# Performance work log

Measured on AMD Instinct MI355X. Metric: run time of the kernel, lower is better.

Reference implementation:

```python
import jax, jax.numpy as jnp
import numpy as np

INPUT_SIZE = 512
HIDDEN_SIZE = 512
BATCH = 16384


def setup_inputs() -> dict:
    key = jax.random.key(0)
    ks = jax.random.split(key, 11)
    stdv = 1.0 / np.sqrt(HIDDEN_SIZE)
    in_dim = INPUT_SIZE + HIDDEN_SIZE

    def unif(k, shape):
        return jax.random.uniform(k, shape, jnp.float32, -stdv, stdv)

    inp = {
        "input_": jax.random.normal(ks[0], (BATCH, INPUT_SIZE), jnp.float32),
        "prev_h": jax.random.normal(ks[1], (BATCH, HIDDEN_SIZE), jnp.float32),
        "prev_c": jax.random.normal(ks[2], (BATCH, HIDDEN_SIZE), jnp.float32),
        # gate weights in torch nn.Linear layout: (out=hidden, in=input+hidden)
        "W_i": unif(ks[3], (HIDDEN_SIZE, in_dim)),
        "b_i": unif(ks[4], (HIDDEN_SIZE,)),
        "W_f": unif(ks[5], (HIDDEN_SIZE, in_dim)),
        "b_f": unif(ks[6], (HIDDEN_SIZE,)),
        "W_g": unif(ks[7], (HIDDEN_SIZE, in_dim)),
        "b_g": unif(ks[8], (HIDDEN_SIZE,)),
        "W_o": unif(ks[9], (HIDDEN_SIZE, in_dim)),
        "b_o": unif(ks[10], (HIDDEN_SIZE,)),
    }
    return inp


def reference(input_, prev_h, prev_c, W_i, b_i, W_f, b_f, W_g, b_g, W_o, b_o):
    # x_stack = cat((prev_h, input_), dim=1)  -> (batch, hidden+input)
    x_stack = jnp.concatenate([prev_h, input_], axis=1)
    # Fuse the four gate GEMMs into one: stack weights along out dim.
    W = jnp.concatenate([W_i, W_f, W_o, W_g], axis=0)          # (4H, H+I)
    b = jnp.concatenate([b_i, b_f, b_o, b_g], axis=0)          # (4H,)
    gates = x_stack @ W.T + b                                   # (batch, 4H)
    H = prev_h.shape[1]
    i = jax.nn.sigmoid(gates[:, 0 * H:1 * H])
    f = jax.nn.sigmoid(gates[:, 1 * H:2 * H])
    o = jax.nn.sigmoid(gates[:, 2 * H:3 * H])
    g = jnp.tanh(gates[:, 3 * H:4 * H])
    c = f * prev_c + i * g
    h = jnp.tanh(c) * o
    return (h, c)
```

## Files before the change

### kernel.cpp

```cpp
#include <hip/hip_runtime.h>
#include <hip/hip_bf16.h>
#include <math.h>

typedef unsigned short u16;

#define BATCH 16384
#define HID   512
#define KDIM  1024
#define BM    128
#define NSTEP 16

typedef __bf16 bf16x8 __attribute__((ext_vector_type(8)));
typedef float  floatx4 __attribute__((ext_vector_type(4)));

__device__ __forceinline__ float fast_sigmoid(float x) {
  return 1.0f / (1.0f + __expf(-x));
}
__device__ __forceinline__ float fast_tanh(float x) {
  float e = __expf(-2.0f * fabsf(x));
  float t = (1.0f - e) / (1.0f + e);
  return x >= 0.0f ? t : -t;
}
__device__ __forceinline__ u16 f2bf(float f) {
  return __builtin_bit_cast(u16, __float2bfloat16(f));
}

__device__ __forceinline__ void barrier_lds_only() {
  asm volatile("s_waitcnt lgkmcnt(0)" ::: "memory");
  __builtin_amdgcn_s_barrier();
  __builtin_amdgcn_sched_barrier(0);
}

__global__ __launch_bounds__(256) void pack_w_kernel(
    const float* __restrict__ Wi, const float* __restrict__ Wf_,
    const float* __restrict__ Wo, const float* __restrict__ Wg,
    u16* __restrict__ Wf) {
  int grow = blockIdx.x;
  int k = threadIdx.x * 4;
  int g = grow >> 9;
  int n = grow & (HID - 1);
  const float* s = g == 0 ? Wi : g == 1 ? Wf_ : g == 2 ? Wo : Wg;
  float4 v = *(const float4*)(s + (size_t)n * KDIM + k);
  ushort4 o;
  o.x = f2bf(v.x); o.y = f2bf(v.y); o.z = f2bf(v.z); o.w = f2bf(v.w);
  size_t d = ((size_t)((g * 32 + (n >> 4)) * 32 + (k >> 5)) * 64 +
              ((k >> 3) & 3) * 16 + (n & 15)) * 8 + (k & 7);
  *(ushort4*)(Wf + d) = o;
}

__global__ __launch_bounds__(512, 2) void lstm_gemm_kernel(
    const float* __restrict__ input_, const float* __restrict__ prev_h,
    const u16* __restrict__ Wf,
    const float* __restrict__ Bi, const float* __restrict__ Bf,
    const float* __restrict__ Bo, const float* __restrict__ Bg,
    const float* __restrict__ prevC, float* __restrict__ out) {
  __shared__ u16 lds[2][8192];

  const int tid = threadIdx.x;
  const int wave = tid >> 6, lane = tid & 63;
  const int lrow = lane & 15, lquad = lane >> 4;
  const int m_block = blockIdx.x * BM;
  const int ntg = blockIdx.y * 8 + wave;

  const int swzf = ((lane & 7) ^ ((lane >> 3) & 7)) * 8;
  const float* xh[2];
  const float* xi[2];
  int lp[2];
#pragma unroll
  for (int i = 0; i < 2; ++i) {
    int li = wave * 2 + i;
    int row = m_block + li * 8 + (lane >> 3);
    xh[i] = prev_h + (size_t)row * HID + swzf;
    xi[i] = input_ + (size_t)row * HID + swzf;
    lp[i] = li * 512 + lane * 8;
  }

  floatx4 acc[4][8];
#pragma unroll
  for (int g = 0; g < 4; ++g)
#pragma unroll
    for (int mt = 0; mt < 8; ++mt)
      acc[g][mt] = (floatx4){0.f, 0.f, 0.f, 0.f};

  float4 r[2][2];
  auto ldX = [&](int S) {
#pragma unroll
    for (int i = 0; i < 2; ++i) {
      const float* base = (S < 8) ? (xh[i] + S * 64) : (xi[i] + (S - 8) * 64);
      r[i][0] = *(const float4*)(base);
      r[i][1] = *(const float4*)(base + 4);
    }
  };

  auto cvtWrite = [&](int buf) {
#pragma unroll
    for (int i = 0; i < 2; ++i) {
      union { u16 u[8]; bf16x8 v; } t;
      t.u[0] = f2bf(r[i][0].x); t.u[1] = f2bf(r[i][0].y);
      t.u[2] = f2bf(r[i][0].z); t.u[3] = f2bf(r[i][0].w);
      t.u[4] = f2bf(r[i][1].x); t.u[5] = f2bf(r[i][1].y);
      t.u[6] = f2bf(r[i][1].z); t.u[7] = f2bf(r[i][1].w);
      *(bf16x8*)(&lds[buf][lp[i]]) = t.v;
    }
  };

  bf16x8 b[2][4];
  auto loadB = [&](int S) {
#pragma unroll
    for (int kk = 0; kk < 2; ++kk)
#pragma unroll
      for (int g = 0; g < 4; ++g)
        b[kk][g] = *(const bf16x8*)(
            Wf + (((size_t)(g * 32 + ntg) * 32 + (S * 2 + kk)) << 9) +
            lane * 8);
  };

  auto compute = [&](int buf) {
    const u16* LA = &lds[buf][0];
    __builtin_amdgcn_s_setprio(1);
#pragma unroll
    for (int kk = 0; kk < 2; ++kk) {
#pragma unroll
      for (int mt = 0; mt < 8; ++mt) {
        bf16x8 a = *(const bf16x8*)
            &LA[(mt * 16 + lrow) * 64 + (((kk * 4 + lquad) ^ (lrow & 7)) * 8)];
#pragma unroll
        for (int g = 0; g < 4; ++g)
          acc[g][mt] = __builtin_amdgcn_mfma_f32_16x16x32_bf16(
              a, b[kk][g], acc[g][mt], 0, 0, 0);
      }
    }
    __builtin_amdgcn_s_setprio(0);
  };

  loadB(0);
  ldX(0);
  cvtWrite(0);
  barrier_lds_only();

  for (int S = 0; S < NSTEP; ++S) {
    const int buf = S & 1;
    if (S + 1 < NSTEP) ldX(S + 1);
    compute(buf);
    if (S + 1 < NSTEP) {
      loadB(S + 1);
      cvtWrite(buf ^ 1);
      barrier_lds_only();
    }
  }

  const int j = ntg * 16 + lrow;
  const float vbi = Bi[j], vbf = Bf[j], vbo = Bo[j], vbg = Bg[j];
  float* outH = out;
  float* outC = out + (size_t)BATCH * HID;
#pragma unroll
  for (int mt = 0; mt < 8; ++mt) {
    int rowb = m_block + mt * 16 + lquad * 4;
#pragma unroll
    for (int rg = 0; rg < 4; ++rg) {
      int row = rowb + rg;
      float gi = fast_sigmoid(acc[0][mt][rg] + vbi);
      float gf = fast_sigmoid(acc[1][mt][rg] + vbf);
      float go = fast_sigmoid(acc[2][mt][rg] + vbo);
      float gg = fast_tanh(acc[3][mt][rg] + vbg);
      float c = gf * prevC[row * HID + j] + gi * gg;
      float h = fast_tanh(c) * go;
      outH[row * HID + j] = h;
      outC[row * HID + j] = c;
    }
  }
}

__global__ void lstm_fallback_kernel(
    const float* __restrict__ input_, const float* __restrict__ prev_h,
    const float* __restrict__ prevC,
    const float* __restrict__ Wi, const float* __restrict__ Bi,
    const float* __restrict__ Wf, const float* __restrict__ Bf,
    const float* __restrict__ Wo, const float* __restrict__ Bo,
    const float* __restrict__ Wg, const float* __restrict__ Bg,
    float* __restrict__ out) {
  int idx = blockIdx.x * blockDim.x + threadIdx.x;
  int b = idx / HID, j = idx % HID;
  if (b >= BATCH) return;
  float si = 0.f, sf = 0.f, so = 0.f, sg = 0.f;
  for (int k = 0; k < KDIM; ++k) {
    float x = (k < HID) ? prev_h[b * HID + k] : input_[b * HID + (k - HID)];
    si += x * Wi[j * KDIM + k];
    sf += x * Wf[j * KDIM + k];
    so += x * Wo[j * KDIM + k];
    sg += x * Wg[j * KDIM + k];
  }
  float gi = fast_sigmoid(si + Bi[j]);
  float gf = fast_sigmoid(sf + Bf[j]);
  float go = fast_sigmoid(so + Bo[j]);
  float gg = fast_tanh(sg + Bg[j]);
  float c = gf * prevC[b * HID + j] + gi * gg;
  out[b * HID + j] = fast_tanh(c) * go;
  out[(size_t)BATCH * HID + b * HID + j] = c;
}

extern "C" void kernel_launch(void* const* d_in, const int* in_sizes, int n_in,
                              void* d_out, int out_size, void* d_ws, size_t ws_size,
                              hipStream_t stream) {
  const float* input_ = (const float*)d_in[0];
  const float* prev_h = (const float*)d_in[1];
  const float* prev_c = (const float*)d_in[2];
  const float* W_i = (const float*)d_in[3];
  const float* b_i = (const float*)d_in[4];
  const float* W_f = (const float*)d_in[5];
  const float* b_f = (const float*)d_in[6];
  const float* W_g = (const float*)d_in[7];
  const float* b_g = (const float*)d_in[8];
  const float* W_o = (const float*)d_in[9];
  const float* b_o = (const float*)d_in[10];
  float* out = (float*)d_out;

  const size_t ws_needed = (size_t)4 * HID * KDIM * sizeof(u16);

  if (ws_size < ws_needed) {
    int total = BATCH * HID;
    lstm_fallback_kernel<<<(total + 255) / 256, 256, 0, stream>>>(
        input_, prev_h, prev_c, W_i, b_i, W_f, b_f, W_o, b_o, W_g, b_g, out);
    return;
  }

  u16* Wfp = (u16*)d_ws;

  pack_w_kernel<<<4 * HID, 256, 0, stream>>>(W_i, W_f, W_o, W_g, Wfp);

  dim3 grid(BATCH / BM, HID / 128);
  lstm_gemm_kernel<<<grid, 512, 0, stream>>>(input_, prev_h, Wfp,
                                             b_i, b_f, b_o, b_g, prev_c, out);
}
```

Measured before the change: 224.7 us.

## Stream activations into an LDS ring with async global_load_lds prefetch

Activation tiles are now loaded with asynchronous global-to-LDS loads into a three-slot fp32 ring, fetched two K-steps ahead. Each step converts them from LDS to bf16 after an explicit vmcnt wait. The grid axes are also swapped so the four column blocks sharing the same rows run next to each other, which should improve L2 reuse of X. The aim is to hide global load latency behind the MFMA work. The trade-off is about 128KB of LDS per block, which likely drops occupancy to one 512-thread block per CU.

```diff
diff --git a/kernel.cpp b/kernel.cpp
--- a/kernel.cpp
+++ b/kernel.cpp
@@ -54,25 +54,21 @@
     const float* __restrict__ Bi, const float* __restrict__ Bf,
     const float* __restrict__ Bo, const float* __restrict__ Bg,
     const float* __restrict__ prevC, float* __restrict__ out) {
-  __shared__ u16 lds[2][8192];
+  __shared__ u16   lbf[2][8192];
+  __shared__ float lring[3][8192];
 
   const int tid = threadIdx.x;
   const int wave = tid >> 6, lane = tid & 63;
   const int lrow = lane & 15, lquad = lane >> 4;
-  const int m_block = blockIdx.x * BM;
-  const int ntg = blockIdx.y * 8 + wave;
-
-  const int swzf = ((lane & 7) ^ ((lane >> 3) & 7)) * 8;
-  const float* xh[2];
-  const float* xi[2];
-  int lp[2];
-#pragma unroll
-  for (int i = 0; i < 2; ++i) {
-    int li = wave * 2 + i;
-    int row = m_block + li * 8 + (lane >> 3);
-    xh[i] = prev_h + (size_t)row * HID + swzf;
-    xi[i] = input_ + (size_t)row * HID + swzf;
-    lp[i] = li * 512 + lane * 8;
+  const int m_block = blockIdx.y * BM;
+  const int ntg = blockIdx.x * 8 + wave;
+
+  int goff[4];
+#pragma unroll
+  for (int i = 0; i < 4; ++i) {
+    int rl = i * 4 + (lane >> 4);
+    int gch = (lane & 15) ^ ((rl & 7) << 1);
+    goff[i] = (m_block + wave * 16 + rl) * HID + gch * 4;
   }
 
   floatx4 acc[4][8];
@@ -82,25 +78,33 @@
     for (int mt = 0; mt < 8; ++mt)
       acc[g][mt] = (floatx4){0.f, 0.f, 0.f, 0.f};
 
-  float4 r[2][2];
-  auto ldX = [&](int S) {
-#pragma unroll
-    for (int i = 0; i < 2; ++i) {
-      const float* base = (S < 8) ? (xh[i] + S * 64) : (xi[i] + (S - 8) * 64);
-      r[i][0] = *(const float4*)(base);
-      r[i][1] = *(const float4*)(base + 4);
-    }
-  };
-
-  auto cvtWrite = [&](int buf) {
-#pragma unroll
-    for (int i = 0; i < 2; ++i) {
+  auto fetchX = [&](int S, int slot) {
+    const float* src = (S < 8) ? prev_h : input_;
+    int colo = (S & 7) * 64;
+#pragma unroll
+    for (int i = 0; i < 4; ++i) {
+      const float* g = src + goff[i] + colo;
+      char* l = (char*)&lring[slot][0] + wave * 4096 + i * 1024;
+      __builtin_amdgcn_global_load_lds(
+          (const __attribute__((address_space(1))) void*)g,
+          (__attribute__((address_space(3))) void*)l, 16, 0, 0);
+    }
+  };
+
+  auto cvt = [&](int slot, int buf) {
+    const int xx = (lane & 7) << 1;
+#pragma unroll
+    for (int pi = 0; pi < 2; ++pi) {
+      int p = lquad + pi * 4;
+      const float* rp = &lring[slot][wave * 1024 + lrow * 64 + (((2 * p) ^ xx) << 2)];
+      float4 v0 = *(const float4*)rp;
+      float4 v1 = *(const float4*)(rp + 4);
       union { u16 u[8]; bf16x8 v; } t;
-      t.u[0] = f2bf(r[i][0].x); t.u[1] = f2bf(r[i][0].y);
-      t.u[2] = f2bf(r[i][0].z); t.u[3] = f2bf(r[i][0].w);
-      t.u[4] = f2bf(r[i][1].x); t.u[5] = f2bf(r[i][1].y);
-      t.u[6] = f2bf(r[i][1].z); t.u[7] = f2bf(r[i][1].w);
-      *(bf16x8*)(&lds[buf][lp[i]]) = t.v;
+      t.u[0] = f2bf(v0.x); t.u[1] = f2bf(v0.y);
+      t.u[2] = f2bf(v0.z); t.u[3] = f2bf(v0.w);
+      t.u[4] = f2bf(v1.x); t.u[5] = f2bf(v1.y);
+      t.u[6] = f2bf(v1.z); t.u[7] = f2bf(v1.w);
+      *(bf16x8*)&lbf[buf][(wave * 16 + lrow) * 64 + ((p ^ (lane & 7)) << 3)] = t.v;
     }
   };
 
@@ -116,7 +120,7 @@
   };
 
   auto compute = [&](int buf) {
-    const u16* LA = &lds[buf][0];
+    const u16* LA = &lbf[buf][0];
     __builtin_amdgcn_s_setprio(1);
 #pragma unroll
     for (int kk = 0; kk < 2; ++kk) {
@@ -133,18 +137,27 @@
     __builtin_amdgcn_s_setprio(0);
   };
 
+  fetchX(0, 0);
+  fetchX(1, 1);
   loadB(0);
-  ldX(0);
-  cvtWrite(0);
+  asm volatile("s_waitcnt vmcnt(12)" ::: "memory");
+  __builtin_amdgcn_sched_barrier(0);
+  cvt(0, 0);
   barrier_lds_only();
 
+#pragma unroll
   for (int S = 0; S < NSTEP; ++S) {
-    const int buf = S & 1;
-    if (S + 1 < NSTEP) ldX(S + 1);
-    compute(buf);
+    compute(S & 1);
     if (S + 1 < NSTEP) {
       loadB(S + 1);
-      cvtWrite(buf ^ 1);
+      if (S + 2 < NSTEP) {
+        fetchX(S + 2, (S + 2) % 3);
+        asm volatile("s_waitcnt vmcnt(12)" ::: "memory");
+      } else {
+        asm volatile("s_waitcnt vmcnt(8)" ::: "memory");
+      }
+      __builtin_amdgcn_sched_barrier(0);
+      cvt((S + 1) % 3, (S + 1) & 1);
       barrier_lds_only();
     }
   }
@@ -228,7 +241,7 @@
 
   pack_w_kernel<<<4 * HID, 256, 0, stream>>>(W_i, W_f, W_o, W_g, Wfp);
 
-  dim3 grid(BATCH / BM, HID / 128);
+  dim3 grid(HID / 128, BATCH / BM);
   lstm_gemm_kernel<<<grid, 512, 0, stream>>>(input_, prev_h, Wfp,
                                              b_i, b_f, b_o, b_g, prev_c, out);
 }
```

Measured after the change: 242.9 us. 8.1% more time.

## Enlarge M tile to 256 with 2x4 wave grid and interleaved barrier schedule

Applied to the files above, without the earlier changes.

Doubles the block's M tile to 256 rows and arranges the 8 waves as a 2x4 grid, so each block covers 4 column groups instead of 8 and each B fragment is reused across more rows. The main loop is split into four MFMA clusters separated by barriers, with global loads of the next X tile and the bf16 LDS writes interleaved between clusters. Block indices are remapped for locality. LDS doubles to 64KB and the frequent barriers could add stall overhead.

```diff
diff --git a/kernel.cpp b/kernel.cpp
--- a/kernel.cpp
+++ b/kernel.cpp
@@ -7,7 +7,7 @@
 #define BATCH 16384
 #define HID   512
 #define KDIM  1024
-#define BM    128
+#define BM    256
 #define NSTEP 16
 
 typedef __bf16 bf16x8 __attribute__((ext_vector_type(8)));
@@ -23,12 +23,6 @@
 }
 __device__ __forceinline__ u16 f2bf(float f) {
   return __builtin_bit_cast(u16, __float2bfloat16(f));
-}
-
-__device__ __forceinline__ void barrier_lds_only() {
-  asm volatile("s_waitcnt lgkmcnt(0)" ::: "memory");
-  __builtin_amdgcn_s_barrier();
-  __builtin_amdgcn_sched_barrier(0);
 }
 
 __global__ __launch_bounds__(256) void pack_w_kernel(
@@ -54,26 +48,25 @@
     const float* __restrict__ Bi, const float* __restrict__ Bf,
     const float* __restrict__ Bo, const float* __restrict__ Bg,
     const float* __restrict__ prevC, float* __restrict__ out) {
-  __shared__ u16 lds[2][8192];
+  __shared__ u16 lbf[2][16384];
 
   const int tid = threadIdx.x;
   const int wave = tid >> 6, lane = tid & 63;
   const int lrow = lane & 15, lquad = lane >> 4;
-  const int m_block = blockIdx.x * BM;
-  const int ntg = blockIdx.y * 8 + wave;
-
-  const int swzf = ((lane & 7) ^ ((lane >> 3) & 7)) * 8;
-  const float* xh[2];
-  const float* xi[2];
-  int lp[2];
-#pragma unroll
-  for (int i = 0; i < 2; ++i) {
-    int li = wave * 2 + i;
-    int row = m_block + li * 8 + (lane >> 3);
-    xh[i] = prev_h + (size_t)row * HID + swzf;
-    xi[i] = input_ + (size_t)row * HID + swzf;
-    lp[i] = li * 512 + lane * 8;
-  }
+  const int wr = wave >> 2, wc = wave & 3;
+
+  int hw = (int)(blockIdx.x + gridDim.x * blockIdx.y);
+  int lid = (hw & 7) * 64 + (hw >> 3);
+  const int m_block = (lid >> 3) * BM;
+  const int ntg = (lid & 7) * 4 + wc;
+
+  const int srow = lane >> 3;
+  const int schunk = (lane & 7) ^ srow;
+  int i_off[4];
+#pragma unroll
+  for (int i = 0; i < 4; ++i)
+    i_off[i] = (m_block + wave * 32 + i * 8 + srow) * HID + schunk * 8;
+  const int lw_off = wave * 2048 + lane * 8;
 
   floatx4 acc[4][8];
 #pragma unroll
@@ -82,26 +75,19 @@
     for (int mt = 0; mt < 8; ++mt)
       acc[g][mt] = (floatx4){0.f, 0.f, 0.f, 0.f};
 
-  float4 r[2][2];
-  auto ldX = [&](int S) {
-#pragma unroll
-    for (int i = 0; i < 2; ++i) {
-      const float* base = (S < 8) ? (xh[i] + S * 64) : (xi[i] + (S - 8) * 64);
-      r[i][0] = *(const float4*)(base);
-      r[i][1] = *(const float4*)(base + 4);
-    }
-  };
-
-  auto cvtWrite = [&](int buf) {
-#pragma unroll
-    for (int i = 0; i < 2; ++i) {
-      union { u16 u[8]; bf16x8 v; } t;
-      t.u[0] = f2bf(r[i][0].x); t.u[1] = f2bf(r[i][0].y);
-      t.u[2] = f2bf(r[i][0].z); t.u[3] = f2bf(r[i][0].w);
-      t.u[4] = f2bf(r[i][1].x); t.u[5] = f2bf(r[i][1].y);
-      t.u[6] = f2bf(r[i][1].z); t.u[7] = f2bf(r[i][1].w);
-      *(bf16x8*)(&lds[buf][lp[i]]) = t.v;
-    }
+  float4 r[4][2];
+  auto ldXi = [&](int t, int i) {
+    const float* bse = ((t < 8) ? prev_h : input_) + i_off[i] + (t & 7) * 64;
+    r[i][0] = *(const float4*)bse;
+    r[i][1] = *(const float4*)(bse + 4);
+  };
+  auto cwi = [&](u16* LW, int i) {
+    union { u16 u[8]; bf16x8 v; } t;
+    t.u[0] = f2bf(r[i][0].x); t.u[1] = f2bf(r[i][0].y);
+    t.u[2] = f2bf(r[i][0].z); t.u[3] = f2bf(r[i][0].w);
+    t.u[4] = f2bf(r[i][1].x); t.u[5] = f2bf(r[i][1].y);
+    t.u[6] = f2bf(r[i][1].z); t.u[7] = f2bf(r[i][1].w);
+    *(bf16x8*)&LW[lw_off + i * 512] = t.v;
   };
 
   bf16x8 b[2][4];
@@ -115,38 +101,91 @@
             lane * 8);
   };
 
-  auto compute = [&](int buf) {
-    const u16* LA = &lds[buf][0];
+  auto rdA = [&](const u16* LA, int kk, int mt) {
+    return *(const bf16x8*)
+        &LA[(wr * 128 + mt * 16 + lrow) * 64 +
+            (((kk * 4 + lquad) ^ (lrow & 7)) * 8)];
+  };
+  auto cluster = [&](bf16x8 a0, bf16x8 a1, bf16x8 a2, bf16x8 a3,
+                     int kk, int mtb) {
     __builtin_amdgcn_s_setprio(1);
 #pragma unroll
-    for (int kk = 0; kk < 2; ++kk) {
-#pragma unroll
-      for (int mt = 0; mt < 8; ++mt) {
-        bf16x8 a = *(const bf16x8*)
-            &LA[(mt * 16 + lrow) * 64 + (((kk * 4 + lquad) ^ (lrow & 7)) * 8)];
-#pragma unroll
-        for (int g = 0; g < 4; ++g)
-          acc[g][mt] = __builtin_amdgcn_mfma_f32_16x16x32_bf16(
-              a, b[kk][g], acc[g][mt], 0, 0, 0);
-      }
+    for (int g = 0; g < 4; ++g) {
+      acc[g][mtb + 0] = __builtin_amdgcn_mfma_f32_16x16x32_bf16(
+          a0, b[kk][g], acc[g][mtb + 0], 0, 0, 0);
+      acc[g][mtb + 1] = __builtin_amdgcn_mfma_f32_16x16x32_bf16(
+          a1, b[kk][g], acc[g][mtb + 1], 0, 0, 0);
+      acc[g][mtb + 2] = __builtin_amdgcn_mfma_f32_16x16x32_bf16(
+          a2, b[kk][g], acc[g][mtb + 2], 0, 0, 0);
+      acc[g][mtb + 3] = __builtin_amdgcn_mfma_f32_16x16x32_bf16(
+          a3, b[kk][g], acc[g][mtb + 3], 0, 0, 0);
     }
     __builtin_amdgcn_s_setprio(0);
   };
 
+  ldXi(0, 0); ldXi(0, 1); ldXi(0, 2); ldXi(0, 3);
+  asm volatile("" ::: "memory");
   loadB(0);
-  ldX(0);
-  cvtWrite(0);
-  barrier_lds_only();
-
-  for (int S = 0; S < NSTEP; ++S) {
-    const int buf = S & 1;
-    if (S + 1 < NSTEP) ldX(S + 1);
-    compute(buf);
-    if (S + 1 < NSTEP) {
-      loadB(S + 1);
-      cvtWrite(buf ^ 1);
-      barrier_lds_only();
-    }
+  asm volatile("s_waitcnt vmcnt(8)" ::: "memory");
+  __builtin_amdgcn_sched_barrier(0);
+  {
+    u16* LW = &lbf[0][0];
+    cwi(LW, 0); cwi(LW, 1); cwi(LW, 2); cwi(LW, 3);
+  }
+  asm volatile("s_waitcnt lgkmcnt(0)" ::: "memory");
+  __builtin_amdgcn_s_barrier();
+
+#pragma unroll 2
+  for (int s = 0; s < NSTEP; ++s) {
+    const u16* LA = &lbf[s & 1][0];
+    u16* LW = &lbf[(s & 1) ^ 1][0];
+    const bool st = (s + 1 < NSTEP);
+    bf16x8 a0, a1, a2, a3;
+
+    a0 = rdA(LA, 0, 0); a1 = rdA(LA, 0, 1);
+    a2 = rdA(LA, 0, 2); a3 = rdA(LA, 0, 3);
+    if (st) { ldXi(s + 1, 0); ldXi(s + 1, 1); }
+    __builtin_amdgcn_s_barrier();
+    asm volatile("s_waitcnt lgkmcnt(0)" ::: "memory");
+    __builtin_amdgcn_sched_barrier(0);
+    cluster(a0, a1, a2, a3, 0, 0);
+    __builtin_amdgcn_s_barrier();
+
+    a0 = rdA(LA, 0, 4); a1 = rdA(LA, 0, 5);
+    a2 = rdA(LA, 0, 6); a3 = rdA(LA, 0, 7);
+    if (st) { ldXi(s + 1, 2); ldXi(s + 1, 3); }
+    __builtin_amdgcn_s_barrier();
+    asm volatile("s_waitcnt lgkmcnt(0)" ::: "memory");
+    __builtin_amdgcn_sched_barrier(0);
+    cluster(a0, a1, a2, a3, 0, 4);
+    __builtin_amdgcn_s_barrier();
+
+    a0 = rdA(LA, 1, 0); a1 = rdA(LA, 1, 1);
+    a2 = rdA(LA, 1, 2); a3 = rdA(LA, 1, 3);
+    if (st) {
+      asm volatile("s_waitcnt vmcnt(4)" ::: "memory");
+      __builtin_amdgcn_sched_barrier(0);
+      cwi(LW, 0); cwi(LW, 1);
+    }
+    __builtin_amdgcn_s_barrier();
+    asm volatile("s_waitcnt lgkmcnt(0)" ::: "memory");
+    __builtin_amdgcn_sched_barrier(0);
+    cluster(a0, a1, a2, a3, 1, 0);
+    __builtin_amdgcn_s_barrier();
+
+    a0 = rdA(LA, 1, 4); a1 = rdA(LA, 1, 5);
+    a2 = rdA(LA, 1, 6); a3 = rdA(LA, 1, 7);
+    if (st) {
+      asm volatile("s_waitcnt vmcnt(0)" ::: "memory");
+      __builtin_amdgcn_sched_barrier(0);
+      cwi(LW, 2); cwi(LW, 3);
+    }
+    __builtin_amdgcn_s_barrier();
+    asm volatile("s_waitcnt lgkmcnt(0)" ::: "memory");
+    __builtin_amdgcn_sched_barrier(0);
+    cluster(a0, a1, a2, a3, 1, 4);
+    if (st) loadB(s + 1);
+    __builtin_amdgcn_s_barrier();
   }
 
   const int j = ntg * 16 + lrow;
@@ -155,7 +194,7 @@
   float* outC = out + (size_t)BATCH * HID;
 #pragma unroll
   for (int mt = 0; mt < 8; ++mt) {
-    int rowb = m_block + mt * 16 + lquad * 4;
+    int rowb = m_block + wr * 128 + mt * 16 + lquad * 4;
 #pragma unroll
     for (int rg = 0; rg < 4; ++rg) {
       int row = rowb + rg;
@@ -228,7 +267,7 @@
 
   pack_w_kernel<<<4 * HID, 256, 0, stream>>>(W_i, W_f, W_o, W_g, Wfp);
 
-  dim3 grid(BATCH / BM, HID / 128);
+  dim3 grid(8, BATCH / BM);
   lstm_gemm_kernel<<<grid, 512, 0, stream>>>(input_, prev_h, Wfp,
                                              b_i, b_f, b_o, b_g, prev_c, out);
 }
```

Result: slower. 288.0 us (+28.2%).

## Double the LDS stage depth to halve block barriers in GEMM loop

Applied to the files above, without the earlier changes.

Each LDS buffer now holds two K-steps of the activation tile, so the main loop runs eight iterations with one barrier each instead of sixteen. Activation global loads are issued further ahead and interleaved between the two half-computes, which gives more time to hide their latency. LDS use per block doubles to 64KB, which may limit occupancy at two blocks per CU. The register-resident B fragments are still reloaded between halves, so the compute order stays the same.

```diff
diff --git a/kernel.cpp b/kernel.cpp
--- a/kernel.cpp
+++ b/kernel.cpp
@@ -9,6 +9,7 @@
 #define KDIM  1024
 #define BM    128
 #define NSTEP 16
+#define NTILE 8
 
 typedef __bf16 bf16x8 __attribute__((ext_vector_type(8)));
 typedef float  floatx4 __attribute__((ext_vector_type(4)));
@@ -54,7 +55,7 @@
     const float* __restrict__ Bi, const float* __restrict__ Bf,
     const float* __restrict__ Bo, const float* __restrict__ Bg,
     const float* __restrict__ prevC, float* __restrict__ out) {
-  __shared__ u16 lds[2][8192];
+  __shared__ u16 lds[2][16384];
 
   const int tid = threadIdx.x;
   const int wave = tid >> 6, lane = tid & 63;
@@ -92,7 +93,8 @@
     }
   };
 
-  auto cvtWrite = [&](int buf) {
+  auto cvtWrite = [&](int buf, int h) {
+    u16* L = &lds[buf][h * 8192];
 #pragma unroll
     for (int i = 0; i < 2; ++i) {
       union { u16 u[8]; bf16x8 v; } t;
@@ -100,7 +102,7 @@
       t.u[2] = f2bf(r[i][0].z); t.u[3] = f2bf(r[i][0].w);
       t.u[4] = f2bf(r[i][1].x); t.u[5] = f2bf(r[i][1].y);
       t.u[6] = f2bf(r[i][1].z); t.u[7] = f2bf(r[i][1].w);
-      *(bf16x8*)(&lds[buf][lp[i]]) = t.v;
+      *(bf16x8*)(&L[lp[i]]) = t.v;
     }
   };
 
@@ -115,8 +117,8 @@
             lane * 8);
   };
 
-  auto compute = [&](int buf) {
-    const u16* LA = &lds[buf][0];
+  auto compute = [&](int buf, int h) {
+    const u16* LA = &lds[buf][h * 8192];
     __builtin_amdgcn_s_setprio(1);
 #pragma unroll
     for (int kk = 0; kk < 2; ++kk) {
@@ -134,17 +136,24 @@
   };
 
   loadB(0);
-  ldX(0);
-  cvtWrite(0);
+  ldX(0); cvtWrite(0, 0);
+  ldX(1); cvtWrite(0, 1);
+  ldX(2);
   barrier_lds_only();
 
-  for (int S = 0; S < NSTEP; ++S) {
-    const int buf = S & 1;
-    if (S + 1 < NSTEP) ldX(S + 1);
-    compute(buf);
-    if (S + 1 < NSTEP) {
-      loadB(S + 1);
-      cvtWrite(buf ^ 1);
+  for (int T = 0; T < NTILE; ++T) {
+    const int buf = T & 1;
+    compute(buf, 0);
+    loadB(2 * T + 1);
+    if (T < NTILE - 1) {
+      cvtWrite(buf ^ 1, 0);
+      ldX(2 * T + 3);
+    }
+    compute(buf, 1);
+    if (T < NTILE - 1) {
+      loadB(2 * T + 2);
+      cvtWrite(buf ^ 1, 1);
+      if (T < NTILE - 2) ldX(2 * T + 4);
       barrier_lds_only();
     }
   }
```

Measured after the change: 227.4 us. About the same (+1.2%).
